# Performance work log

Hardware: AMD Instinct MI355X
Metric: run time of the kernel (lower is better)

The kernel has to match this reference:

```python
import jax, jax.numpy as jnp
import numpy as np

G_ZERO_INIT = 32.0  # g initialized to log2(g0^2 - g0)


def setup_inputs() -> dict:
    key = jax.random.key(0)
    k1, k2, k3 = jax.random.split(key, 3)
    B, L, D = 64, 16384, 64
    query = jax.random.normal(k1, (B, 1, D), dtype=jnp.float32)
    keys = jax.random.normal(k2, (B, L, D), dtype=jnp.float32)
    values = jax.random.normal(k3, (B, L, 1), dtype=jnp.float32)
    g = jnp.asarray(np.log2(G_ZERO_INIT**2 - G_ZERO_INIT), dtype=jnp.float32)
    return {"query": query, "keys": keys, "values": values, "g": g, "k": 256}


def reference(query, keys, values, g, k):
    # cosine similarity between query (B,1,D) and keys (B,L,D) -> (B,L)
    qn = query / jnp.linalg.norm(query, axis=-1, keepdims=True)
    kn = keys / jnp.linalg.norm(keys, axis=-1, keepdims=True)
    similarity = jnp.einsum("bqd,bld->bl", qn, kn) * g  # (B, L)
    # top-k select + batched gather of values
    top_sim, idx = jax.lax.top_k(similarity, k)          # (B, k) each
    values_sel = jnp.take_along_axis(values, idx[:, :, None], axis=1)  # (B, k, 1)
    weights = jax.nn.softmax(top_sim, axis=-1)           # (B, k)
    return values_sel, weights
```

## Files before the change

### kernel.cpp

```cpp
#include <hip/hip_runtime.h>
#include <math.h>

#define BATCH 64
#define LSEQ  16384
#define DIM   64
#define KSEL  256

__global__ __launch_bounds__(256) void sim_kernel(
    const float* __restrict__ q,
    const float* __restrict__ keys,
    const float* __restrict__ gp,
    double* __restrict__ sims)
{
    const int b     = blockIdx.x >> 6;
    const int chunk = blockIdx.x & 63;
    const int t  = threadIdx.x;
    const int j  = t & 15;
    const int rl = t >> 4;

    const float4* q4 = reinterpret_cast<const float4*>(q) + b * 16;
    float4 qv = q4[j];
    const double qx = qv.x, qy = qv.y, qz = qv.z, qw = qv.w;
    double qss = qx*qx + qy*qy + qz*qz + qw*qw;
    #pragma unroll
    for (int m = 1; m < 16; m <<= 1) qss += __shfl_xor(qss, m);
    const double scale = (double)gp[0] / sqrt(qss);

    __shared__ double local[256];
    const float4* k4 = reinterpret_cast<const float4*>(keys) + (size_t)b * LSEQ * 16;
    const int row_base = chunk * 256;

    for (int it = 0; it < 16; ++it) {
        const int row = row_base + it * 16 + rl;
        float4 kv = k4[row * 16 + j];
        const double kx = kv.x, ky = kv.y, kz = kv.z, kw = kv.w;
        double dot = qx*kx + qy*ky + qz*kz + qw*kw;
        double kss = kx*kx + ky*ky + kz*kz + kw*kw;
        #pragma unroll
        for (int m = 1; m < 16; m <<= 1) {
            dot += __shfl_xor(dot, m);
            kss += __shfl_xor(kss, m);
        }
        if (j == 0) local[it * 16 + rl] = scale * dot / sqrt(kss);
    }
    __syncthreads();
    sims[(size_t)b * LSEQ + row_base + t] = local[t];
}

__global__ __launch_bounds__(256, 1) void topk_kernel(
    const double* __restrict__ sims,
    const float* __restrict__ values,
    float* __restrict__ out)
{
    const int b = blockIdx.x;
    const int t = threadIdx.x;
    const double* s = sims + (size_t)b * LSEQ;

    unsigned long long skey[64];
    #pragma unroll
    for (int it = 0; it < 64; ++it) {
        unsigned long long u =
            (unsigned long long)__double_as_longlong(s[it * 256 + t]);
        skey[it] = (u >> 63) ? ~u : (u | 0x8000000000000000ull);
    }

    __shared__ unsigned hist[256];
    __shared__ unsigned scan[256];
    __shared__ ulonglong2 cand[512];
    __shared__ unsigned sh_prefix, sh_mask, sh_k, ccount;

    if (t == 0) { sh_prefix = 0u; sh_mask = 0u; sh_k = KSEL; ccount = 0u; }

    for (int p = 0; p < 4; ++p) {
        const int shift = 24 - 8 * p;
        hist[t] = 0u;
        __syncthreads();
        const unsigned prefix = sh_prefix;
        const unsigned mask   = sh_mask;
        const unsigned kcur   = sh_k;
        #pragma unroll
        for (int it = 0; it < 64; ++it) {
            unsigned hi = (unsigned)(skey[it] >> 32);
            if (((hi ^ prefix) & mask) == 0u)
                atomicAdd(&hist[(hi >> shift) & 255u], 1u);
        }
        __syncthreads();
        scan[t] = hist[t];
        __syncthreads();
        #pragma unroll
        for (int off = 1; off < 256; off <<= 1) {
            unsigned v = (t + off < 256) ? scan[t + off] : 0u;
            __syncthreads();
            scan[t] += v;
            __syncthreads();
        }
        if (scan[t] >= kcur && (t == 255 || scan[t + 1] < kcur)) {
            sh_prefix = prefix | ((unsigned)t << shift);
            sh_mask   = mask | (0xFFu << shift);
            sh_k      = kcur - ((t == 255) ? 0u : scan[t + 1]);
        }
        __syncthreads();
    }
    const unsigned T32 = sh_prefix;

    #pragma unroll
    for (int it = 0; it < 64; ++it) {
        unsigned long long key = skey[it];
        if ((unsigned)(key >> 32) >= T32) {
            unsigned pos = atomicAdd(&ccount, 1u);
            if (pos < 512u) {
                unsigned idx = (unsigned)(it * 256 + t);
                cand[pos] = make_ulonglong2(
                    key, (unsigned long long)(0xFFFFFFFFu - idx));
            }
        }
    }
    __syncthreads();
    const unsigned total = ccount < 512u ? ccount : 512u;
    for (int i = t; i < 512; i += 256)
        if ((unsigned)i >= total) cand[i] = make_ulonglong2(0ull, 0ull);

    for (int size = 2; size <= 512; size <<= 1) {
        for (int stride = size >> 1; stride > 0; stride >>= 1) {
            __syncthreads();
            int i  = ((t & ~(stride - 1)) << 1) | (t & (stride - 1));
            int jj = i + stride;
            bool up = ((i & size) == 0);
            ulonglong2 a = cand[i], c = cand[jj];
            bool agt = (a.x > c.x) || (a.x == c.x && a.y > c.y);
            if (agt == up) { cand[i] = c; cand[jj] = a; }
        }
    }
    __syncthreads();

    ulonglong2 v = cand[511 - t];
    unsigned idx = 0xFFFFFFFFu - (unsigned)v.y;
    unsigned long long ub = (v.x & 0x8000000000000000ull)
                          ? (v.x ^ 0x8000000000000000ull) : ~v.x;
    double sv = __longlong_as_double((long long)ub);

    ulonglong2 vm = cand[511];
    unsigned long long um = (vm.x & 0x8000000000000000ull)
                          ? (vm.x ^ 0x8000000000000000ull) : ~vm.x;
    double fm = __longlong_as_double((long long)um);

    double e = exp(sv - fm);
    double esum = e;
    #pragma unroll
    for (int m = 1; m < 64; m <<= 1) esum += __shfl_xor(esum, m);
    __shared__ double wsum[4];
    if ((t & 63) == 0) wsum[t >> 6] = esum;
    __syncthreads();
    const double tot = wsum[0] + wsum[1] + wsum[2] + wsum[3];

    out[b * KSEL + t]                = values[(size_t)b * LSEQ + idx];
    out[BATCH * KSEL + b * KSEL + t] = (float)(e / tot);
}

extern "C" void kernel_launch(void* const* d_in, const int* in_sizes, int n_in,
                              void* d_out, int out_size, void* d_ws, size_t ws_size,
                              hipStream_t stream)
{
    const float* q      = (const float*)d_in[0];
    const float* keys   = (const float*)d_in[1];
    const float* values = (const float*)d_in[2];
    const float* g      = (const float*)d_in[3];
    float* out   = (float*)d_out;
    double* sims = (double*)d_ws;

    sim_kernel<<<dim3(BATCH * (LSEQ / 256)), dim3(256), 0, stream>>>(q, keys, g, sims);
    topk_kernel<<<dim3(BATCH), dim3(256), 0, stream>>>(sims, values, out);
}
```

Before: 403.1 us.

## Fuse similarity and top-k into one kernel with float prefilter and double rescoring

Merges the two kernels into one 1024-thread block per batch row. Each row gets a float32 proxy score (dot*|dot|/kss), stored as 32-bit keys in shared memory. A two-pass 8-bit radix histogram picks a padded threshold of 384 candidates, and only those candidates are recomputed in double precision before the bitonic sort and softmax. This removes the double-precision sims round trip through global memory and most of the FP64 work. In exchange, only 64 blocks run (one per batch), which may leave many CUs idle while streaming the 256MB of keys, and the float prefilter could mis-rank entries near the threshold.

```diff
diff --git a/kernel.cpp b/kernel.cpp
--- a/kernel.cpp
+++ b/kernel.cpp
@@ -5,169 +5,235 @@
 #define LSEQ  16384
 #define DIM   64
 #define KSEL  256
-
-__global__ __launch_bounds__(256) void sim_kernel(
+#define KPAD  384
+#define NCAND 512
+
+
+__device__ __forceinline__ void reduce_hist(unsigned (*histR)[256],
+                                            unsigned* hist, int t)
+{
+    if (t < 256) {
+        unsigned h = 0;
+        #pragma unroll
+        for (int r = 0; r < 8; ++r) h += histR[r][t];
+        hist[t] = h;
+    }
+    __syncthreads();
+}
+
+__device__ __forceinline__ void suffix_scan_256(const unsigned* hist,
+                                                unsigned* scan,
+                                                unsigned* wbase, int t)
+{
+    const int lane = t & 63, w4 = t >> 6;
+    unsigned v = (t < 256) ? hist[t] : 0u;
+    #pragma unroll
+    for (int off = 1; off < 64; off <<= 1) {
+        unsigned u2 = __shfl_down(v, off);
+        if (lane + off < 64) v += u2;
+    }
+    if (t < 256 && lane == 0) wbase[w4] = v;
+    __syncthreads();
+    if (t < 256) {
+        for (int w = w4 + 1; w < 4; ++w) v += wbase[w];
+        scan[t] = v;
+    }
+    __syncthreads();
+}
+
+__global__ __launch_bounds__(1024) void fused_topk_kernel(
     const float* __restrict__ q,
     const float* __restrict__ keys,
+    const float* __restrict__ values,
     const float* __restrict__ gp,
-    double* __restrict__ sims)
-{
-    const int b     = blockIdx.x >> 6;
-    const int chunk = blockIdx.x & 63;
-    const int t  = threadIdx.x;
-    const int j  = t & 15;
-    const int rl = t >> 4;
-
-    const float4* q4 = reinterpret_cast<const float4*>(q) + b * 16;
-    float4 qv = q4[j];
+    float* __restrict__ out)
+{
+    const int b = blockIdx.x;
+    const int t = threadIdx.x;
+
+    __shared__ unsigned   skey[LSEQ];
+    __shared__ unsigned   histR[8][256];
+    __shared__ unsigned   hist[256];
+    __shared__ unsigned   scan[256];
+    __shared__ unsigned   wbase[4];
+    __shared__ unsigned   cidx[NCAND];
+    __shared__ ulonglong2 cand[NCAND];
+    __shared__ double     wsum[4];
+    __shared__ unsigned   sh_hi8, sh_k, sh_t16, ccount;
+
+    ((unsigned*)histR)[t]        = 0u;
+    ((unsigned*)histR)[t + 1024] = 0u;
+    if (t == 0) { ccount = 0u; sh_hi8 = 0u; sh_k = KPAD; sh_t16 = 0u; }
+    __syncthreads();
+
+    const int lane4 = t & 3;
+    const int rbase = t >> 2;
+    const float4* k4 = reinterpret_cast<const float4*>(keys)
+                     + (size_t)b * LSEQ * (DIM / 4);
+    const float4* q4 = reinterpret_cast<const float4*>(q) + b * (DIM / 4);
+
+    float4 qa = q4[lane4 * 4 + 0];
+    float4 qb = q4[lane4 * 4 + 1];
+    float4 qc = q4[lane4 * 4 + 2];
+    float4 qd = q4[lane4 * 4 + 3];
+    const int rep = (t >> 2) & 7;
+
+    #pragma unroll 2
+    for (int it = 0; it < 64; ++it) {
+        const int row = it * 256 + rbase;
+        const float4* kp = k4 + row * 16 + lane4 * 4;
+        float4 ka = kp[0], kb = kp[1], kc = kp[2], kd = kp[3];
+
+        float dot = qa.x*ka.x + qa.y*ka.y + qa.z*ka.z + qa.w*ka.w
+                  + qb.x*kb.x + qb.y*kb.y + qb.z*kb.z + qb.w*kb.w
+                  + qc.x*kc.x + qc.y*kc.y + qc.z*kc.z + qc.w*kc.w
+                  + qd.x*kd.x + qd.y*kd.y + qd.z*kd.z + qd.w*kd.w;
+        float kss = ka.x*ka.x + ka.y*ka.y + ka.z*ka.z + ka.w*ka.w
+                  + kb.x*kb.x + kb.y*kb.y + kb.z*kb.z + kb.w*kb.w
+                  + kc.x*kc.x + kc.y*kc.y + kc.z*kc.z + kc.w*kc.w
+                  + kd.x*kd.x + kd.y*kd.y + kd.z*kd.z + kd.w*kd.w;
+        dot += __shfl_xor(dot, 1); dot += __shfl_xor(dot, 2);
+        kss += __shfl_xor(kss, 1); kss += __shfl_xor(kss, 2);
+
+        if (lane4 == 0) {
+            float s = dot * fabsf(dot) / kss;
+            unsigned u = __float_as_uint(s);
+            unsigned key = (u >> 31) ? ~u : (u | 0x80000000u);
+            skey[row] = key;
+            atomicAdd(&histR[rep][key >> 24], 1u);
+        }
+    }
+    __syncthreads();
+
+    reduce_hist(histR, hist, t);
+    suffix_scan_256(hist, scan, wbase, t);
+    if (t < 256 && scan[t] >= KPAD && (t == 255 || scan[t + 1] < KPAD)) {
+        sh_hi8 = (unsigned)t;
+        sh_k   = KPAD - ((t == 255) ? 0u : scan[t + 1]);
+    }
+    __syncthreads();
+
+    ((unsigned*)histR)[t]        = 0u;
+    ((unsigned*)histR)[t + 1024] = 0u;
+    __syncthreads();
+    const unsigned hi8  = sh_hi8;
+    const unsigned kcur = sh_k;
+    #pragma unroll
+    for (int it = 0; it < 16; ++it) {
+        unsigned key = skey[it * 1024 + t];
+        if ((key >> 24) == hi8)
+            atomicAdd(&histR[t & 7][(key >> 16) & 255u], 1u);
+    }
+    __syncthreads();
+    reduce_hist(histR, hist, t);
+    suffix_scan_256(hist, scan, wbase, t);
+    if (t < 256 && scan[t] >= kcur && (t == 255 || scan[t + 1] < kcur))
+        sh_t16 = (hi8 << 8) | (unsigned)t;
+    __syncthreads();
+    const unsigned T16 = sh_t16;
+
+    #pragma unroll
+    for (int it = 0; it < 16; ++it) {
+        const int l = it * 1024 + t;
+        unsigned key = skey[l];
+        if ((key >> 16) >= T16) {
+            unsigned pos = atomicAdd(&ccount, 1u);
+            if (pos < NCAND) cidx[pos] = (unsigned)l;
+        }
+    }
+    __syncthreads();
+    const unsigned total = (ccount < (unsigned)NCAND) ? ccount : (unsigned)NCAND;
+
+    const int j = t & 15;
+    const float4 qv = q4[j];
     const double qx = qv.x, qy = qv.y, qz = qv.z, qw = qv.w;
     double qss = qx*qx + qy*qy + qz*qz + qw*qw;
     #pragma unroll
     for (int m = 1; m < 16; m <<= 1) qss += __shfl_xor(qss, m);
     const double scale = (double)gp[0] / sqrt(qss);
 
-    __shared__ double local[256];
-    const float4* k4 = reinterpret_cast<const float4*>(keys) + (size_t)b * LSEQ * 16;
-    const int row_base = chunk * 256;
-
-    for (int it = 0; it < 16; ++it) {
-        const int row = row_base + it * 16 + rl;
-        float4 kv = k4[row * 16 + j];
-        const double kx = kv.x, ky = kv.y, kz = kv.z, kw = kv.w;
-        double dot = qx*kx + qy*ky + qz*kz + qw*kw;
-        double kss = kx*kx + ky*ky + kz*kz + kw*kw;
-        #pragma unroll
-        for (int m = 1; m < 16; m <<= 1) {
-            dot += __shfl_xor(dot, m);
-            kss += __shfl_xor(kss, m);
-        }
-        if (j == 0) local[it * 16 + rl] = scale * dot / sqrt(kss);
-    }
-    __syncthreads();
-    sims[(size_t)b * LSEQ + row_base + t] = local[t];
-}
-
-__global__ __launch_bounds__(256, 1) void topk_kernel(
-    const double* __restrict__ sims,
-    const float* __restrict__ values,
-    float* __restrict__ out)
-{
-    const int b = blockIdx.x;
-    const int t = threadIdx.x;
-    const double* s = sims + (size_t)b * LSEQ;
-
-    unsigned long long skey[64];
-    #pragma unroll
-    for (int it = 0; it < 64; ++it) {
-        unsigned long long u =
-            (unsigned long long)__double_as_longlong(s[it * 256 + t]);
-        skey[it] = (u >> 63) ? ~u : (u | 0x8000000000000000ull);
-    }
-
-    __shared__ unsigned hist[256];
-    __shared__ unsigned scan[256];
-    __shared__ ulonglong2 cand[512];
-    __shared__ unsigned sh_prefix, sh_mask, sh_k, ccount;
-
-    if (t == 0) { sh_prefix = 0u; sh_mask = 0u; sh_k = KSEL; ccount = 0u; }
-
-    for (int p = 0; p < 4; ++p) {
-        const int shift = 24 - 8 * p;
-        hist[t] = 0u;
-        __syncthreads();
-        const unsigned prefix = sh_prefix;
-        const unsigned mask   = sh_mask;
-        const unsigned kcur   = sh_k;
-        #pragma unroll
-        for (int it = 0; it < 64; ++it) {
-            unsigned hi = (unsigned)(skey[it] >> 32);
-            if (((hi ^ prefix) & mask) == 0u)
-                atomicAdd(&hist[(hi >> shift) & 255u], 1u);
-        }
-        __syncthreads();
-        scan[t] = hist[t];
-        __syncthreads();
-        #pragma unroll
-        for (int off = 1; off < 256; off <<= 1) {
-            unsigned v = (t + off < 256) ? scan[t + off] : 0u;
-            __syncthreads();
-            scan[t] += v;
-            __syncthreads();
-        }
-        if (scan[t] >= kcur && (t == 255 || scan[t + 1] < kcur)) {
-            sh_prefix = prefix | ((unsigned)t << shift);
-            sh_mask   = mask | (0xFFu << shift);
-            sh_k      = kcur - ((t == 255) ? 0u : scan[t + 1]);
-        }
-        __syncthreads();
-    }
-    const unsigned T32 = sh_prefix;
-
-    #pragma unroll
-    for (int it = 0; it < 64; ++it) {
-        unsigned long long key = skey[it];
-        if ((unsigned)(key >> 32) >= T32) {
-            unsigned pos = atomicAdd(&ccount, 1u);
-            if (pos < 512u) {
-                unsigned idx = (unsigned)(it * 256 + t);
-                cand[pos] = make_ulonglong2(
-                    key, (unsigned long long)(0xFFFFFFFFu - idx));
+    const int cslot = t >> 4;
+    for (int sweep = 0; sweep < NCAND / 64; ++sweep) {
+        const int cc = sweep * 64 + cslot;
+        if (cc < (int)total) {
+            const int row = (int)cidx[cc];
+            float4 kv = k4[row * 16 + j];
+            const double kx = kv.x, ky = kv.y, kz = kv.z, kw = kv.w;
+            double dot = qx*kx + qy*ky + qz*kz + qw*kw;
+            double kss = kx*kx + ky*ky + kz*kz + kw*kw;
+            #pragma unroll
+            for (int m = 1; m < 16; m <<= 1) {
+                dot += __shfl_xor(dot, m);
+                kss += __shfl_xor(kss, m);
             }
-        }
-    }
-    __syncthreads();
-    const unsigned total = ccount < 512u ? ccount : 512u;
-    for (int i = t; i < 512; i += 256)
-        if ((unsigned)i >= total) cand[i] = make_ulonglong2(0ull, 0ull);
-
-    for (int size = 2; size <= 512; size <<= 1) {
+            if (j == 0) {
+                double sim = scale * dot / sqrt(kss);
+                unsigned long long u =
+                    (unsigned long long)__double_as_longlong(sim);
+                unsigned long long k64 =
+                    (u >> 63) ? ~u : (u | 0x8000000000000000ull);
+                cand[cc] = make_ulonglong2(
+                    k64, (unsigned long long)(0xFFFFFFFFu - (unsigned)row));
+            }
+        } else if (j == 0) {
+            cand[cc] = make_ulonglong2(0ull, 0ull);
+        }
+    }
+    __syncthreads();
+
+    for (int size = 2; size <= NCAND; size <<= 1) {
         for (int stride = size >> 1; stride > 0; stride >>= 1) {
             __syncthreads();
-            int i  = ((t & ~(stride - 1)) << 1) | (t & (stride - 1));
-            int jj = i + stride;
-            bool up = ((i & size) == 0);
-            ulonglong2 a = cand[i], c = cand[jj];
-            bool agt = (a.x > c.x) || (a.x == c.x && a.y > c.y);
-            if (agt == up) { cand[i] = c; cand[jj] = a; }
-        }
-    }
-    __syncthreads();
-
-    ulonglong2 v = cand[511 - t];
-    unsigned idx = 0xFFFFFFFFu - (unsigned)v.y;
-    unsigned long long ub = (v.x & 0x8000000000000000ull)
-                          ? (v.x ^ 0x8000000000000000ull) : ~v.x;
-    double sv = __longlong_as_double((long long)ub);
-
-    ulonglong2 vm = cand[511];
-    unsigned long long um = (vm.x & 0x8000000000000000ull)
-                          ? (vm.x ^ 0x8000000000000000ull) : ~vm.x;
-    double fm = __longlong_as_double((long long)um);
-
-    double e = exp(sv - fm);
-    double esum = e;
-    #pragma unroll
-    for (int m = 1; m < 64; m <<= 1) esum += __shfl_xor(esum, m);
-    __shared__ double wsum[4];
-    if ((t & 63) == 0) wsum[t >> 6] = esum;
-    __syncthreads();
-    const double tot = wsum[0] + wsum[1] + wsum[2] + wsum[3];
-
-    out[b * KSEL + t]                = values[(size_t)b * LSEQ + idx];
-    out[BATCH * KSEL + b * KSEL + t] = (float)(e / tot);
+            if (t < 256) {
+                int i  = ((t & ~(stride - 1)) << 1) | (t & (stride - 1));
+                int jj = i + stride;
+                bool up = ((i & size) == 0);
+                ulonglong2 a = cand[i], c = cand[jj];
+                bool agt = (a.x > c.x) || (a.x == c.x && a.y > c.y);
+                if (agt == up) { cand[i] = c; cand[jj] = a; }
+            }
+        }
+    }
+    __syncthreads();
+
+    double e = 0.0;
+    unsigned idx = 0u;
+    if (t < 256) {
+        ulonglong2 v = cand[511 - t];
+        idx = 0xFFFFFFFFu - (unsigned)v.y;
+        unsigned long long ub = (v.x & 0x8000000000000000ull)
+                              ? (v.x ^ 0x8000000000000000ull) : ~v.x;
+        double sv = __longlong_as_double((long long)ub);
+
+        ulonglong2 vm = cand[511];
+        unsigned long long um = (vm.x & 0x8000000000000000ull)
+                              ? (vm.x ^ 0x8000000000000000ull) : ~vm.x;
+        double fm = __longlong_as_double((long long)um);
+
+        e = exp(sv - fm);
+        double esum = e;
+        #pragma unroll
+        for (int m = 1; m < 64; m <<= 1) esum += __shfl_xor(esum, m);
+        if ((t & 63) == 0) wsum[t >> 6] = esum;
+    }
+    __syncthreads();
+    if (t < 256) {
+        const double tot = wsum[0] + wsum[1] + wsum[2] + wsum[3];
+        out[b * KSEL + t]                = values[(size_t)b * LSEQ + idx];
+        out[BATCH * KSEL + b * KSEL + t] = (float)(e / tot);
+    }
 }
 
 extern "C" void kernel_launch(void* const* d_in, const int* in_sizes, int n_in,
                               void* d_out, int out_size, void* d_ws, size_t ws_size,
                               hipStream_t stream)
 {
+    (void)d_ws; (void)ws_size;
     const float* q      = (const float*)d_in[0];
     const float* keys   = (const float*)d_in[1];
     const float* values = (const float*)d_in[2];
     const float* g      = (const float*)d_in[3];
-    float* out   = (float*)d_out;
-    double* sims = (double*)d_ws;
-
-    sim_kernel<<<dim3(BATCH * (LSEQ / 256)), dim3(256), 0, stream>>>(q, keys, g, sims);
-    topk_kernel<<<dim3(BATCH), dim3(256), 0, stream>>>(sims, values, out);
-}
+    float* out = (float*)d_out;
+
+    fused_topk_kernel<<<dim3(BATCH), dim3(1024), 0, stream>>>(q, keys, values, g, out);
+}
```

After: 450.5 us. +11.8%, slower.
